# Performance work log

Hardware: AMD Instinct MI355X
Metric: run time of the kernel (lower is better)

Reference implementation:

```python
import jax, jax.numpy as jnp
import numpy as np

ALPHA = 0.9          # alpha_mem
THRESHOLD = 1.0
WINDOW = 1.0         # module-level `window`; spike fn receives threshold*window
MEM_SUBTRACT = THRESHOLD  # membrane_subtract defaults to threshold


@jax.custom_vjp
def spike(v):
    # sinabs ThresholdSubtract forward: multiple spikes per step via floor division
    return jnp.where(v > 0, jnp.floor(v / THRESHOLD), 0.0)

def _spike_fwd(v):
    return spike(v), v

def _spike_bwd(v, g):
    # surrogate gradient: boxcar heaviside(v - (threshold - window)) / threshold
    grad = (v >= (THRESHOLD - THRESHOLD * WINDOW)).astype(g.dtype) / THRESHOLD
    return (g * grad,)

spike.defvjp(_spike_fwd, _spike_bwd)


def setup_inputs() -> dict:
    key = jax.random.key(0)
    k1, k2 = jax.random.split(key, 2)
    B, T, N = 32, 1000, 1024
    input_current = jax.random.normal(k1, (B, T, N), dtype=jnp.float32)
    w_rec = jax.random.normal(k2, (N, N), dtype=jnp.float32) * 0.02  # Linear weight [out, in]
    b_rec = jnp.zeros((N,), dtype=jnp.float32)
    return {"input_current": input_current, "w_rec": w_rec, "b_rec": b_rec}


def reference(input_current, w_rec, b_rec):
    B, T, N = input_current.shape

    def step(carry, x_t):
        state, rec = carry                      # [B, N] each
        total = x_t + rec                       # recurrent feedback added to input
        act = spike(state)                      # spikes from state BEFORE integration (1-step delay)
        state = state - act * MEM_SUBTRACT      # membrane subtract after spiking
        state = state * ALPHA + (1.0 - ALPHA) * total  # leaky integration
        rec = act @ w_rec.T + b_rec             # recurrent GEMM for next step
        return (state, rec), act

    state0 = jnp.zeros((B, N), dtype=input_current.dtype)
    rec0 = jnp.zeros((B, N), dtype=input_current.dtype)
    xs = jnp.swapaxes(input_current, 0, 1)      # [T, B, N]
    _, spikes = jax.lax.scan(step, (state0, rec0), xs)
    return jnp.swapaxes(spikes, 0, 1)           # [B, T, N]
```

## Files before the change

kernel.cpp:

```cpp
#include <hip/hip_runtime.h>
#include <cstdint>
#include <cstddef>

#define B_       32
#define T_       1000
#define N_       1024
#define THREADS_ 256
#define WAVES_   4
#define CHUNK_   8
#define NCHUNK_  (T_ / CHUNK_)
#define ZBLOCKS_ 2048

typedef float v4f __attribute__((ext_vector_type(4)));

__device__ __forceinline__ void barrier_lds() {
  __asm__ volatile("s_waitcnt lgkmcnt(0)\n\ts_barrier" ::: "memory");
}

#define VMWAIT(N) __asm__ volatile("s_waitcnt vmcnt(" #N ")" ::: "memory")

typedef const __attribute__((address_space(1))) void* gas_ptr;
typedef __attribute__((address_space(3))) void*       las_ptr;

__global__ __launch_bounds__(THREADS_, 1)
void lif_fused(const float* __restrict__ x, const float* __restrict__ w,
               const float* __restrict__ brec_g, float* __restrict__ out,
               unsigned long long* __restrict__ ws_rec,
               unsigned int* __restrict__ ws_cnt, int cap)
{
  if (blockIdx.x >= B_) {
    const size_t n4 = (size_t)B_ * T_ * N_ / 4;
    size_t i = (size_t)(blockIdx.x - B_) * THREADS_ + threadIdx.x;
    const size_t stride = (size_t)(gridDim.x - B_) * THREADS_;
    v4f* o4 = (v4f*)out;
    v4f z = (v4f)(0.f);
    for (; i < n4; i += stride) __builtin_nontemporal_store(z, &o4[i]);
    return;
  }

  const int b    = blockIdx.x;
  const int tid  = threadIdx.x;
  const int lane = tid & 63;
  const int wv   = tid >> 6;
  const int n0   = tid << 2;

  __shared__ float xbuf0[CHUNK_][N_];
  __shared__ float xbuf1[CHUNK_][N_];
  __shared__ float xbuf2[CHUNK_][N_];
  __shared__ unsigned long long s_cmask[2][WAVES_];
  __shared__ unsigned long long s_mask [2][WAVES_];
  __shared__ v4f                s_val  [2][THREADS_];
  __shared__ unsigned int       s_spkcnt;

  if (tid == 0) s_spkcnt = 0;

  const float* xg = x + (size_t)b * T_ * N_ + (wv << 8) + (lane << 2);

  v4f state = (v4f)(0.f);
  v4f rec   = (v4f)(0.f);
  const v4f brec = *(const v4f*)(brec_g + n0);

#define ISSUE_LDS(bufv, c)                                                   \
  do {                                                                       \
    const float* _g = xg + (size_t)(c) * (CHUNK_ * N_);                      \
    _Pragma("unroll")                                                        \
    for (int _k = 0; _k < CHUNK_; ++_k)                                      \
      __builtin_amdgcn_global_load_lds((gas_ptr)(_g + (size_t)_k * N_),      \
                                       (las_ptr)&bufv[_k][wv << 8],          \
                                       16, 0, 0);                            \
  } while (0)

  auto process = [&](const float* xrow, int c) {
    v4f xs[CHUNK_];
#pragma unroll
    for (int k = 0; k < CHUNK_; ++k)
      xs[k] = *(const v4f*)(xrow + (size_t)k * N_ + n0);

    v4f st = state;
    v4f r  = rec;
    v4f cmax = st;
#pragma unroll
    for (int k = 0; k < CHUNK_; ++k) {
      cmax.x = fmaxf(cmax.x, st.x);
      cmax.y = fmaxf(cmax.y, st.y);
      cmax.z = fmaxf(cmax.z, st.z);
      cmax.w = fmaxf(cmax.w, st.w);
      v4f t = xs[k] + r;
      st = st * 0.9f + 0.1f * t;
      r = brec;
    }
    float m = fmaxf(fmaxf(cmax.x, cmax.y), fmaxf(cmax.z, cmax.w));
    int any = (m >= 1.0f);

    const int p = c & 1;
    unsigned long long wm = __ballot(any);
    if (lane == 0) s_cmask[p][wv] = wm;
    barrier_lds();
    unsigned long long anyblk =
        s_cmask[p][0] | s_cmask[p][1] | s_cmask[p][2] | s_cmask[p][3];

    if (anyblk == 0ULL) {
      state = st;
      rec   = brec;
      return;
    }

    st = state;
    r  = rec;
#pragma unroll 1
    for (int k = 0; k < CHUNK_; ++k) {
      const int q = k & 1;
      float tx = xs[k].x + r.x, ty = xs[k].y + r.y,
            tz = xs[k].z + r.z, tw = xs[k].w + r.w;
      float ax = (st.x > 0.f) ? floorf(st.x) : 0.f;
      float ay = (st.y > 0.f) ? floorf(st.y) : 0.f;
      float az = (st.z > 0.f) ? floorf(st.z) : 0.f;
      float aw = (st.w > 0.f) ? floorf(st.w) : 0.f;
      int ms = (ax != 0.f) | (ay != 0.f) | (az != 0.f) | (aw != 0.f);
      if (ms) {
        v4f v; v.x = ax; v.y = ay; v.z = az; v.w = aw;
        s_val[q][tid] = v;
        unsigned int off = (unsigned int)((c * CHUNK_ + k) * N_ + n0);
        float av[4] = {ax, ay, az, aw};
#pragma unroll
        for (int e = 0; e < 4; ++e) {
          if (av[e] != 0.f) {
            unsigned int idx = atomicAdd(&s_spkcnt, 1u);
            if ((int)idx < cap)
              ws_rec[(size_t)b * cap + idx] =
                  ((unsigned long long)(off + e) << 32) |
                  (unsigned long long)__float_as_uint(av[e]);
          }
        }
      }
      unsigned long long sm = __ballot(ms);
      if (lane == 0) s_mask[q][wv] = sm;
      st.x = (st.x - ax) * 0.9f + 0.1f * tx;
      st.y = (st.y - ay) * 0.9f + 0.1f * ty;
      st.z = (st.z - az) * 0.9f + 0.1f * tz;
      st.w = (st.w - aw) * 0.9f + 0.1f * tw;
      barrier_lds();
      v4f racc = brec;
#pragma unroll 1
      for (int w2 = 0; w2 < WAVES_; ++w2) {
        unsigned long long mm = s_mask[q][w2];
        while (mm) {
          int l = __builtin_ctzll(mm);
          mm &= mm - 1;
          int j = (w2 << 6) + l;
          v4f v = s_val[q][j];
          int jn = j << 2;
          if (v.x != 0.f) {
            racc.x += v.x * w[(size_t)(n0 + 0) * N_ + jn];
            racc.y += v.x * w[(size_t)(n0 + 1) * N_ + jn];
            racc.z += v.x * w[(size_t)(n0 + 2) * N_ + jn];
            racc.w += v.x * w[(size_t)(n0 + 3) * N_ + jn];
          }
          if (v.y != 0.f) {
            int j1 = jn + 1;
            racc.x += v.y * w[(size_t)(n0 + 0) * N_ + j1];
            racc.y += v.y * w[(size_t)(n0 + 1) * N_ + j1];
            racc.z += v.y * w[(size_t)(n0 + 2) * N_ + j1];
            racc.w += v.y * w[(size_t)(n0 + 3) * N_ + j1];
          }
          if (v.z != 0.f) {
            int j2 = jn + 2;
            racc.x += v.z * w[(size_t)(n0 + 0) * N_ + j2];
            racc.y += v.z * w[(size_t)(n0 + 1) * N_ + j2];
            racc.z += v.z * w[(size_t)(n0 + 2) * N_ + j2];
            racc.w += v.z * w[(size_t)(n0 + 3) * N_ + j2];
          }
          if (v.w != 0.f) {
            int j3 = jn + 3;
            racc.x += v.w * w[(size_t)(n0 + 0) * N_ + j3];
            racc.y += v.w * w[(size_t)(n0 + 1) * N_ + j3];
            racc.z += v.w * w[(size_t)(n0 + 2) * N_ + j3];
            racc.w += v.w * w[(size_t)(n0 + 3) * N_ + j3];
          }
        }
      }
      r = racc;
    }
    state = st;
    rec   = r;
  };

  const float* x0row = &xbuf0[0][0];
  const float* x1row = &xbuf1[0][0];
  const float* x2row = &xbuf2[0][0];

  ISSUE_LDS(xbuf0, 0);
  ISSUE_LDS(xbuf1, 1);

  int c = 0;
#pragma unroll 1
  for (int t3 = 0; t3 < 41; ++t3) {
    ISSUE_LDS(xbuf2, c + 2);
    VMWAIT(16);
    process(x0row, c);
    ISSUE_LDS(xbuf0, c + 3);
    VMWAIT(16);
    process(x1row, c + 1);
    ISSUE_LDS(xbuf1, c + 4);
    VMWAIT(16);
    process(x2row, c + 2);
    c += 3;
  }
  VMWAIT(8);
  process(x0row, 123);
  VMWAIT(0);
  process(x1row, 124);

  __syncthreads();
  if (tid == 0) ws_cnt[b] = s_spkcnt;
#undef ISSUE_LDS
}

__global__ void scatter_spikes(const unsigned long long* __restrict__ rec,
                               const unsigned int* __restrict__ cnt,
                               float* __restrict__ out, int cap)
{
  int b = blockIdx.x;
  unsigned int n = cnt[b];
  if ((int)n > cap) n = cap;
  for (unsigned int i = threadIdx.x; i < n; i += blockDim.x) {
    unsigned long long r = rec[(size_t)b * cap + i];
    unsigned int off = (unsigned int)(r >> 32);
    float v = __uint_as_float((unsigned int)r);
    out[(size_t)b * (T_ * N_) + off] = v;
  }
}

extern "C" void kernel_launch(void* const* d_in, const int* in_sizes, int n_in,
                              void* d_out, int out_size, void* d_ws, size_t ws_size,
                              hipStream_t stream) {
  const float* x  = (const float*)d_in[0];
  const float* w  = (const float*)d_in[1];
  const float* br = (const float*)d_in[2];
  float* out = (float*)d_out;

  int cap = 4096;
  size_t need = (size_t)B_ * cap * 8 + B_ * 4;
  if (ws_size < need && ws_size > 256)
    cap = (int)((ws_size - 256) / ((size_t)B_ * 8));
  unsigned long long* rec = (unsigned long long*)d_ws;
  unsigned int* cnt = (unsigned int*)((char*)d_ws + (size_t)B_ * cap * 8);

  lif_fused<<<B_ + ZBLOCKS_, THREADS_, 0, stream>>>(x, w, br, out, rec, cnt, cap);
  scatter_spikes<<<B_, THREADS_, 0, stream>>>(rec, cnt, out, cap);
}
```

Measured before the change: 358.1 us.

## Split block into producer and consumer waves for chunk prefetch ring

Doubles the recurrent block to 512 threads, with 4 dedicated producer waves issuing global-to-LDS loads into a 3-slot ring while 4 consumer waves run the speculative no-spike check and the spiking replay. Producers stay in lockstep by matching the consumers' barriers, including 8 dummy barriers on replay chunks. The aim is to take load issue and vmcnt waits off the consumer critical path. The zeroing grid is halved to 1024 blocks. The cost is more threads per recurrent CU and a harder barrier protocol, which could deadlock if the barrier counts ever diverge.

```diff
diff --git a/kernel.cpp b/kernel.cpp
--- a/kernel.cpp
+++ b/kernel.cpp
@@ -5,11 +5,12 @@
 #define B_       32
 #define T_       1000
 #define N_       1024
-#define THREADS_ 256
-#define WAVES_   4
+#define THREADS_ 512
+#define CWAVES_  4
 #define CHUNK_   8
-#define NCHUNK_  (T_ / CHUNK_)
-#define ZBLOCKS_ 2048
+#define NCHUNK_  125
+#define RING_    3
+#define ZBLOCKS_ 1024
 
 typedef float v4f __attribute__((ext_vector_type(4)));
 
@@ -21,6 +22,13 @@
 
 typedef const __attribute__((address_space(1))) void* gas_ptr;
 typedef __attribute__((address_space(3))) void*       las_ptr;
+
+__device__ __forceinline__ v4f vmax4(v4f a, v4f b) {
+  v4f r;
+  r.x = fmaxf(a.x, b.x); r.y = fmaxf(a.y, b.y);
+  r.z = fmaxf(a.z, b.z); r.w = fmaxf(a.w, b.w);
+  return r;
+}
 
 __global__ __launch_bounds__(THREADS_, 1)
 void lif_fused(const float* __restrict__ x, const float* __restrict__ w,
@@ -42,76 +50,47 @@
   const int tid  = threadIdx.x;
   const int lane = tid & 63;
   const int wv   = tid >> 6;
+  const bool is_prod = (wv >= CWAVES_);
+  const int pw   = wv - CWAVES_;
   const int n0   = tid << 2;
 
-  __shared__ float xbuf0[CHUNK_][N_];
-  __shared__ float xbuf1[CHUNK_][N_];
-  __shared__ float xbuf2[CHUNK_][N_];
-  __shared__ unsigned long long s_cmask[2][WAVES_];
-  __shared__ unsigned long long s_mask [2][WAVES_];
-  __shared__ v4f                s_val  [2][THREADS_];
+  __shared__ float xring[RING_][CHUNK_][N_];
+  __shared__ unsigned long long s_cmask[2][CWAVES_];
+  __shared__ unsigned long long s_mask [2][CWAVES_];
+  __shared__ v4f                s_val  [2][256];
   __shared__ unsigned int       s_spkcnt;
 
-  if (tid == 0) s_spkcnt = 0;
-
-  const float* xg = x + (size_t)b * T_ * N_ + (wv << 8) + (lane << 2);
+  const float* xb = x + (size_t)b * (T_ * N_);
+
+  auto issue_chunk = [&](int cc) {
+    const int slot = cc % RING_;
+    const float* src = xb + (size_t)cc * (CHUNK_ * N_) + (lane << 2);
+#pragma unroll
+    for (int rr = 0; rr < 2; ++rr) {
+      const int row = (pw << 1) + rr;
+      const float* rs = src + row * N_;
+      float* ld = &xring[slot][row][0];
+#pragma unroll
+      for (int q = 0; q < 4; ++q)
+        __builtin_amdgcn_global_load_lds((gas_ptr)(rs + q * 256),
+                                         (las_ptr)(ld + q * 256), 16, 0, 0);
+    }
+  };
 
   v4f state = (v4f)(0.f);
   v4f rec   = (v4f)(0.f);
-  const v4f brec = *(const v4f*)(brec_g + n0);
-
-#define ISSUE_LDS(bufv, c)                                                   \
-  do {                                                                       \
-    const float* _g = xg + (size_t)(c) * (CHUNK_ * N_);                      \
-    _Pragma("unroll")                                                        \
-    for (int _k = 0; _k < CHUNK_; ++_k)                                      \
-      __builtin_amdgcn_global_load_lds((gas_ptr)(_g + (size_t)_k * N_),      \
-                                       (las_ptr)&bufv[_k][wv << 8],          \
-                                       16, 0, 0);                            \
-  } while (0)
-
-  auto process = [&](const float* xrow, int c) {
-    v4f xs[CHUNK_];
-#pragma unroll
-    for (int k = 0; k < CHUNK_; ++k)
-      xs[k] = *(const v4f*)(xrow + (size_t)k * N_ + n0);
-
+  v4f brec  = (v4f)(0.f);
+  if (!is_prod) brec = *(const v4f*)(brec_g + n0);
+
+  auto replay = [&](int i) {
     v4f st = state;
     v4f r  = rec;
-    v4f cmax = st;
-#pragma unroll
-    for (int k = 0; k < CHUNK_; ++k) {
-      cmax.x = fmaxf(cmax.x, st.x);
-      cmax.y = fmaxf(cmax.y, st.y);
-      cmax.z = fmaxf(cmax.z, st.z);
-      cmax.w = fmaxf(cmax.w, st.w);
-      v4f t = xs[k] + r;
-      st = st * 0.9f + 0.1f * t;
-      r = brec;
-    }
-    float m = fmaxf(fmaxf(cmax.x, cmax.y), fmaxf(cmax.z, cmax.w));
-    int any = (m >= 1.0f);
-
-    const int p = c & 1;
-    unsigned long long wm = __ballot(any);
-    if (lane == 0) s_cmask[p][wv] = wm;
-    barrier_lds();
-    unsigned long long anyblk =
-        s_cmask[p][0] | s_cmask[p][1] | s_cmask[p][2] | s_cmask[p][3];
-
-    if (anyblk == 0ULL) {
-      state = st;
-      rec   = brec;
-      return;
-    }
-
-    st = state;
-    r  = rec;
+    const float* xr = &xring[i % RING_][0][0];
 #pragma unroll 1
     for (int k = 0; k < CHUNK_; ++k) {
       const int q = k & 1;
-      float tx = xs[k].x + r.x, ty = xs[k].y + r.y,
-            tz = xs[k].z + r.z, tw = xs[k].w + r.w;
+      v4f xv = *(const v4f*)(xr + (size_t)k * N_ + n0);
+      float tx = xv.x + r.x, ty = xv.y + r.y, tz = xv.z + r.z, tw = xv.w + r.w;
       float ax = (st.x > 0.f) ? floorf(st.x) : 0.f;
       float ay = (st.y > 0.f) ? floorf(st.y) : 0.f;
       float az = (st.z > 0.f) ? floorf(st.z) : 0.f;
@@ -120,7 +99,7 @@
       if (ms) {
         v4f v; v.x = ax; v.y = ay; v.z = az; v.w = aw;
         s_val[q][tid] = v;
-        unsigned int off = (unsigned int)((c * CHUNK_ + k) * N_ + n0);
+        unsigned int off = (unsigned int)((i * CHUNK_ + k) * N_ + n0);
         float av[4] = {ax, ay, az, aw};
 #pragma unroll
         for (int e = 0; e < 4; ++e) {
@@ -142,7 +121,7 @@
       barrier_lds();
       v4f racc = brec;
 #pragma unroll 1
-      for (int w2 = 0; w2 < WAVES_; ++w2) {
+      for (int w2 = 0; w2 < CWAVES_; ++w2) {
         unsigned long long mm = s_mask[q][w2];
         while (mm) {
           int l = __builtin_ctzll(mm);
@@ -185,35 +164,73 @@
     rec   = r;
   };
 
-  const float* x0row = &xbuf0[0][0];
-  const float* x1row = &xbuf1[0][0];
-  const float* x2row = &xbuf2[0][0];
-
-  ISSUE_LDS(xbuf0, 0);
-  ISSUE_LDS(xbuf1, 1);
-
-  int c = 0;
-#pragma unroll 1
-  for (int t3 = 0; t3 < 41; ++t3) {
-    ISSUE_LDS(xbuf2, c + 2);
-    VMWAIT(16);
-    process(x0row, c);
-    ISSUE_LDS(xbuf0, c + 3);
-    VMWAIT(16);
-    process(x1row, c + 1);
-    ISSUE_LDS(xbuf1, c + 4);
-    VMWAIT(16);
-    process(x2row, c + 2);
-    c += 3;
-  }
-  VMWAIT(8);
-  process(x0row, 123);
-  VMWAIT(0);
-  process(x1row, 124);
+  if (tid == 0) s_spkcnt = 0;
+  if (is_prod) {
+    issue_chunk(0);
+    issue_chunk(1);
+    VMWAIT(8);
+  }
+  barrier_lds();
+
+#pragma unroll 1
+  for (int i = 0; i < NCHUNK_; ++i) {
+    v4f st, cmax;
+    if (is_prod) {
+      if (i + 2 < NCHUNK_) {
+        issue_chunk(i + 2);
+        VMWAIT(8);
+      } else {
+        VMWAIT(0);
+      }
+    } else {
+      const float* xr = &xring[i % RING_][0][0];
+      v4f x0 = *(const v4f*)(xr + 0 * N_ + n0);
+      v4f x1 = *(const v4f*)(xr + 1 * N_ + n0);
+      v4f x2 = *(const v4f*)(xr + 2 * N_ + n0);
+      v4f x3 = *(const v4f*)(xr + 3 * N_ + n0);
+      v4f x4 = *(const v4f*)(xr + 4 * N_ + n0);
+      v4f x5 = *(const v4f*)(xr + 5 * N_ + n0);
+      v4f x6 = *(const v4f*)(xr + 6 * N_ + n0);
+      v4f x7 = *(const v4f*)(xr + 7 * N_ + n0);
+      st = state;
+      v4f rr = rec;
+      cmax = state;
+#define SPEC_STEP(xf)                                                        \
+      do {                                                                   \
+        cmax = vmax4(cmax, st);                                              \
+        v4f _t = (xf) + rr;                                                  \
+        st = st * 0.9f + 0.1f * _t;                                          \
+        rr = brec;                                                           \
+      } while (0)
+      SPEC_STEP(x0); SPEC_STEP(x1); SPEC_STEP(x2); SPEC_STEP(x3);
+      SPEC_STEP(x4); SPEC_STEP(x5); SPEC_STEP(x6); SPEC_STEP(x7);
+#undef SPEC_STEP
+      float m = fmaxf(fmaxf(cmax.x, cmax.y), fmaxf(cmax.z, cmax.w));
+      int any = (m >= 1.0f);
+      unsigned long long wm = __ballot(any);
+      if (lane == 0) s_cmask[i & 1][wv] = wm;
+    }
+
+    barrier_lds();
+
+    unsigned long long anyblk =
+        s_cmask[i & 1][0] | s_cmask[i & 1][1] |
+        s_cmask[i & 1][2] | s_cmask[i & 1][3];
+
+    if (anyblk == 0ULL) {
+      if (!is_prod) { state = st; rec = brec; }
+    } else {
+      if (!is_prod) {
+        replay(i);
+      } else {
+#pragma unroll 1
+        for (int k = 0; k < CHUNK_; ++k) barrier_lds();
+      }
+    }
+  }
 
   __syncthreads();
   if (tid == 0) ws_cnt[b] = s_spkcnt;
-#undef ISSUE_LDS
 }
 
 __global__ void scatter_spikes(const unsigned long long* __restrict__ rec,
```

After: 333.8 us. -6.8%, faster.
